# Performance work log

Hardware: AMD Instinct MI355X
Metric: run time of the kernel (lower is better)

Reference implementation:

```python
import jax, jax.numpy as jnp
import numpy as np

DIM = 1024
N_EXPERTS = 8
TOP_K = 2
B, S = 2, 1024


def setup_inputs() -> dict:
    key = jax.random.key(0)
    ks = jax.random.split(key, 4)
    scale = 0.02
    return {
        "u_t": jax.random.normal(ks[0], (B, S, DIM), dtype=jnp.float32),
        "centroids": jax.random.normal(ks[1], (N_EXPERTS, DIM), dtype=jnp.float32),
        "score_biases": jnp.zeros((N_EXPERTS,), dtype=jnp.float32),
        "W1": jax.random.normal(ks[2], (N_EXPERTS, DIM, 4 * DIM), dtype=jnp.float32) * scale,
        "b1": jnp.zeros((N_EXPERTS, 4 * DIM), dtype=jnp.float32),
        "W2": jax.random.normal(ks[3], (N_EXPERTS, 4 * DIM, DIM), dtype=jnp.float32) * scale,
        "b2": jnp.zeros((N_EXPERTS, DIM), dtype=jnp.float32),
    }


def reference(u_t, centroids, score_biases, W1, b1, W2, b2):
    Bs, Ss, dim = u_t.shape
    T = Bs * Ss
    N = centroids.shape[0]
    K = TOP_K

    u_flat = u_t.reshape(T, dim)
    scores = u_flat @ centroids.T + score_biases          # [T, N]
    gate = jax.nn.softmax(scores, axis=-1)                # [T, N]
    topk_vals, topk_idx = jax.lax.top_k(gate, K)          # [T, K]

    flat_idx = topk_idx.reshape(-1)                       # [T*K]

    # load-violation stats (no grad path; pure counts)
    perfect_load = K * T / N
    f_i = jnp.zeros((N,), dtype=jnp.float32).at[flat_idx].add(1.0)
    maxvio = (jnp.max(f_i) - perfect_load) / perfect_load

    # Grouped MLP expressed as dense per-expert compute over all tokens,
    # then combined with a sparse [T, N] gate matrix (same math as masked dispatch).
    h = jax.nn.relu(jnp.einsum("td,ndh->nth", u_flat, W1) + b1[:, None, :])  # [N, T, 4*dim]
    expert_outs = jnp.einsum("nth,nhd->ntd", h, W2) + b2[:, None, :]          # [N, T, dim]

    rows = jnp.repeat(jnp.arange(T), K)
    combine_w = jnp.zeros((T, N), dtype=topk_vals.dtype).at[rows, flat_idx].add(topk_vals.reshape(-1))
    out = jnp.einsum("tn,ntd->td", combine_w, expert_outs).reshape(Bs, Ss, dim)
    return (out, maxvio)
```

## Files before the change

kernel.cpp:

```cpp
#include <hip/hip_runtime.h>
#include <hip/hip_bf16.h>

#define T_TOK 2048
#define DIMS  1024
#define HID   4096
#define NE    8

typedef __bf16 bf16x8 __attribute__((ext_vector_type(8)));
typedef float  f32x4  __attribute__((ext_vector_type(4)));

__device__ __forceinline__ unsigned short f2bf(float f) {
  unsigned u = __float_as_uint(f);
  u += 0x7FFFu + ((u >> 16) & 1u);
  return (unsigned short)(u >> 16);
}

__device__ __forceinline__ void g2l16(const void* g, void* l) {
  __builtin_amdgcn_global_load_lds((const __attribute__((address_space(1))) void*)g,
                                   (__attribute__((address_space(3))) void*)l,
                                   16, 0, 0);
}

__global__ __launch_bounds__(256) void k_zero(int* cnt) {
  if (threadIdx.x < NE) cnt[threadIdx.x] = 0;
}

__global__ __launch_bounds__(256) void k_route(const float* __restrict__ u,
    const float* __restrict__ cent, const float* __restrict__ sbias,
    int* __restrict__ topk_idx, float* __restrict__ topk_val, int* __restrict__ cnt) {
  int wave = threadIdx.x >> 6;
  int lane = threadIdx.x & 63;
  int t = blockIdx.x * 4 + wave;
  const float* ur = u + (size_t)t * DIMS;
  float p[NE];
#pragma unroll
  for (int n = 0; n < NE; n++) p[n] = 0.f;
#pragma unroll
  for (int ch = 0; ch < 4; ch++) {
    int d = ch * 256 + lane * 4;
    float4 uv = *(const float4*)(ur + d);
#pragma unroll
    for (int n = 0; n < NE; n++) {
      float4 cv = *(const float4*)(cent + n * DIMS + d);
      p[n] += uv.x * cv.x + uv.y * cv.y + uv.z * cv.z + uv.w * cv.w;
    }
  }
#pragma unroll
  for (int n = 0; n < NE; n++) {
#pragma unroll
    for (int o = 32; o > 0; o >>= 1) p[n] += __shfl_xor(p[n], o);
  }
  if (lane == 0) {
    float g[NE];
    float m = -1e30f;
#pragma unroll
    for (int n = 0; n < NE; n++) { g[n] = p[n] + sbias[n]; m = fmaxf(m, g[n]); }
    float sum = 0.f;
#pragma unroll
    for (int n = 0; n < NE; n++) { g[n] = expf(g[n] - m); sum += g[n]; }
    float inv = 1.f / sum;
#pragma unroll
    for (int n = 0; n < NE; n++) g[n] *= inv;
    int i0 = 0;
#pragma unroll
    for (int n = 1; n < NE; n++) if (g[n] > g[i0]) i0 = n;
    int i1 = (i0 == 0) ? 1 : 0;
#pragma unroll
    for (int n = 0; n < NE; n++) if (n != i0 && g[n] > g[i1]) i1 = n;
    topk_idx[2 * t] = i0;     topk_idx[2 * t + 1] = i1;
    topk_val[2 * t] = g[i0];  topk_val[2 * t + 1] = g[i1];
    atomicAdd(&cnt[i0], 1);
    atomicAdd(&cnt[i1], 1);
  }
}

__global__ __launch_bounds__(64) void k_finalize(const int* __restrict__ cnt,
    int* __restrict__ offs, int* __restrict__ cursor, float* __restrict__ maxvio) {
  if (threadIdx.x == 0) {
    int o = 0, mx = 0;
#pragma unroll
    for (int n = 0; n < NE; n++) { offs[n] = o; o += cnt[n]; mx = max(mx, cnt[n]); }
    maxvio[0] = ((float)mx - 512.f) / 512.f;
#pragma unroll
    for (int n = 0; n < NE; n++) cursor[n] = 0;
  }
}

__global__ __launch_bounds__(256) void k_place(const int* __restrict__ topk_idx,
    const int* __restrict__ offs, int* __restrict__ cursor,
    int* __restrict__ rowtok, int* __restrict__ pairpos) {
  int t = blockIdx.x * 256 + threadIdx.x;
  if (t >= T_TOK) return;
#pragma unroll
  for (int k = 0; k < 2; k++) {
    int e = topk_idx[2 * t + k];
    int pos = atomicAdd(&cursor[e], 1);
    rowtok[offs[e] + pos] = t;
    pairpos[2 * t + k] = offs[e] + pos;
  }
}

__global__ __launch_bounds__(256) void k_cvt_u(const float* __restrict__ u,
                                               unsigned short* __restrict__ ub) {
  int i = (blockIdx.x * 256 + threadIdx.x) * 8;
  float4 a = *(const float4*)(u + i);
  float4 b = *(const float4*)(u + i + 4);
  union { unsigned short us[8]; uint4 v; } r;
  r.us[0] = f2bf(a.x); r.us[1] = f2bf(a.y); r.us[2] = f2bf(a.z); r.us[3] = f2bf(a.w);
  r.us[4] = f2bf(b.x); r.us[5] = f2bf(b.y); r.us[6] = f2bf(b.z); r.us[7] = f2bf(b.w);
  *(uint4*)(ub + i) = r.v;
}

__global__ __launch_bounds__(256) void k_cvt_w(const float* __restrict__ W,
    unsigned short* __restrict__ out, int R, int C) {
  __shared__ float tile[64][65];
  int e = blockIdx.z;
  size_t base = (size_t)e * R * C;
  int r0 = blockIdx.y * 64, c0 = blockIdx.x * 64;
  int tr  = threadIdx.x >> 4;
  int tc4 = (threadIdx.x & 15) * 4;
#pragma unroll
  for (int it = 0; it < 4; it++) {
    int row = tr + it * 16;
    float4 v = *(const float4*)(W + base + (size_t)(r0 + row) * C + c0 + tc4);
    tile[row][tc4] = v.x; tile[row][tc4 + 1] = v.y; tile[row][tc4 + 2] = v.z; tile[row][tc4 + 3] = v.w;
  }
  __syncthreads();
  int c = threadIdx.x >> 2;
  int seg = (threadIdx.x & 3) * 16;
  union { unsigned short us[8]; uint4 v; } r;
#pragma unroll
  for (int half = 0; half < 2; half++) {
#pragma unroll
    for (int i = 0; i < 8; i++) r.us[i] = f2bf(tile[seg + half * 8 + i][c]);
    *(uint4*)(out + base + (size_t)(c0 + c) * R + r0 + seg + half * 8) = r.v;
  }
}

#define BM 128
#define BN 128
#define BK 64

__global__ __launch_bounds__(256) void k_gemm1(const unsigned short* __restrict__ ub,
    const unsigned short* __restrict__ w1t, const float* __restrict__ b1,
    const int* __restrict__ rowtok, const int* __restrict__ cnts, const int* __restrict__ offs,
    unsigned short* __restrict__ h) {
  int e = blockIdx.z;
  int cnt = cnts[e];
  int m0 = blockIdx.y * BM;
  if (m0 >= cnt) return;
  int off = offs[e];
  int n0 = blockIdx.x * BN;
  __shared__ __align__(16) unsigned char smem[32768];

  int tid = threadIdx.x;
  int lane = tid & 63;
  int wm = (tid >> 7) & 1;
  int wn = (tid >> 6) & 1;
  int srow = tid >> 3;
  int cp = tid & 7;
  const unsigned short* gA[4];
  const unsigned short* gB[4];
#pragma unroll
  for (int a = 0; a < 4; a++) {
    int r = a * 32 + srow;
    int c = cp ^ (r & 7);
    int pr = min(off + m0 + r, off + cnt - 1);
    int tok = rowtok[pr];
    gA[a] = ub + (size_t)tok * DIMS + c * 8;
    gB[a] = w1t + ((size_t)e * HID + (n0 + r)) * DIMS + c * 8;
  }
  int wboff = __builtin_amdgcn_readfirstlane((tid >> 6) << 10);
  f32x4 acc[4][4];
  f32x4 zz = {0.f, 0.f, 0.f, 0.f};
#pragma unroll
  for (int i = 0; i < 4; i++)
#pragma unroll
    for (int j = 0; j < 4; j++) acc[i][j] = zz;

  int lane15 = lane & 15, quad = lane >> 4, l7 = lane & 7;
  unsigned aRowOff = (unsigned)((wm * 64 + lane15) * 128);
  unsigned bRowOff = (unsigned)(16384 + (wn * 64 + lane15) * 128);

#pragma unroll 1
  for (int k0 = 0; k0 < DIMS; k0 += BK) {
#pragma unroll
    for (int a = 0; a < 4; a++) g2l16(gA[a] + k0, smem + a * 4096 + wboff);
#pragma unroll
    for (int a = 0; a < 4; a++) g2l16(gB[a] + k0, smem + 16384 + a * 4096 + wboff);
    __syncthreads();
#pragma unroll
    for (int s = 0; s < 2; s++) {
      unsigned cpf = (unsigned)(((s * 4 + quad) ^ l7) * 16);
      bf16x8 af[4], bfr[4];
#pragma unroll
      for (int i = 0; i < 4; i++) af[i] = *(const bf16x8*)(smem + aRowOff + i * 2048 + cpf);
#pragma unroll
      for (int j = 0; j < 4; j++) bfr[j] = *(const bf16x8*)(smem + bRowOff + j * 2048 + cpf);
#pragma unroll
      for (int i = 0; i < 4; i++)
#pragma unroll
        for (int j = 0; j < 4; j++)
          acc[i][j] = __builtin_amdgcn_mfma_f32_16x16x32_bf16(af[i], bfr[j], acc[i][j], 0, 0, 0);
    }
    __syncthreads();
  }
  float b1v[4];
#pragma unroll
  for (int j = 0; j < 4; j++) b1v[j] = b1[e * HID + n0 + wn * 64 + j * 16 + lane15];
#pragma unroll
  for (int i = 0; i < 4; i++) {
#pragma unroll
    for (int r = 0; r < 4; r++) {
      int mrow = m0 + wm * 64 + i * 16 + quad * 4 + r;
      if (mrow < cnt) {
        size_t hrow = (size_t)(off + mrow) * HID;
#pragma unroll
        for (int j = 0; j < 4; j++) {
          int col = n0 + wn * 64 + j * 16 + lane15;
          float v = fmaxf(acc[i][j][r] + b1v[j], 0.f);
          h[hrow + col] = f2bf(v);
        }
      }
    }
  }
}

__global__ __launch_bounds__(256) void k_gemm2(const unsigned short* __restrict__ hbuf,
    const unsigned short* __restrict__ w2t, const float* __restrict__ b2,
    const int* __restrict__ cnts, const int* __restrict__ offs,
    float* __restrict__ pout, int KC) {
  int z = blockIdx.z;
  int e = z & 7;
  int sp = z >> 3;
  int cnt = cnts[e];
  int m0 = blockIdx.y * BM;
  if (m0 >= cnt) return;
  int off = offs[e];
  int n0 = blockIdx.x * BN;
  __shared__ __align__(16) unsigned char smem[32768];

  int tid = threadIdx.x;
  int lane = tid & 63;
  int wm = (tid >> 7) & 1;
  int wn = (tid >> 6) & 1;
  int srow = tid >> 3;
  int cp = tid & 7;
  const unsigned short* gA[4];
  const unsigned short* gB[4];
#pragma unroll
  for (int a = 0; a < 4; a++) {
    int r = a * 32 + srow;
    int c = cp ^ (r & 7);
    int pr = min(off + m0 + r, off + cnt - 1);
    gA[a] = hbuf + (size_t)pr * HID + c * 8;
    gB[a] = w2t + ((size_t)e * DIMS + (n0 + r)) * HID + c * 8;
  }
  int wboff = __builtin_amdgcn_readfirstlane((tid >> 6) << 10);
  f32x4 acc[4][4];
  f32x4 zz = {0.f, 0.f, 0.f, 0.f};
#pragma unroll
  for (int i = 0; i < 4; i++)
#pragma unroll
    for (int j = 0; j < 4; j++) acc[i][j] = zz;

  int lane15 = lane & 15, quad = lane >> 4, l7 = lane & 7;
  unsigned aRowOff = (unsigned)((wm * 64 + lane15) * 128);
  unsigned bRowOff = (unsigned)(16384 + (wn * 64 + lane15) * 128);

  int kbeg = sp * KC, kend = kbeg + KC;
#pragma unroll 1
  for (int k0 = kbeg; k0 < kend; k0 += BK) {
#pragma unroll
    for (int a = 0; a < 4; a++) g2l16(gA[a] + k0, smem + a * 4096 + wboff);
#pragma unroll
    for (int a = 0; a < 4; a++) g2l16(gB[a] + k0, smem + 16384 + a * 4096 + wboff);
    __syncthreads();
#pragma unroll
    for (int s = 0; s < 2; s++) {
      unsigned cpf = (unsigned)(((s * 4 + quad) ^ l7) * 16);
      bf16x8 af[4], bfr[4];
#pragma unroll
      for (int i = 0; i < 4; i++) af[i] = *(const bf16x8*)(smem + aRowOff + i * 2048 + cpf);
#pragma unroll
      for (int j = 0; j < 4; j++) bfr[j] = *(const bf16x8*)(smem + bRowOff + j * 2048 + cpf);
#pragma unroll
      for (int i = 0; i < 4; i++)
#pragma unroll
        for (int j = 0; j < 4; j++)
          acc[i][j] = __builtin_amdgcn_mfma_f32_16x16x32_bf16(af[i], bfr[j], acc[i][j], 0, 0, 0);
    }
    __syncthreads();
  }
  float b2v[4];
#pragma unroll
  for (int j = 0; j < 4; j++)
    b2v[j] = (sp == 0) ? b2[e * DIMS + n0 + wn * 64 + j * 16 + lane15] : 0.f;
  float* pme = pout + (size_t)sp * T_TOK * 2 * DIMS;
#pragma unroll
  for (int i = 0; i < 4; i++) {
#pragma unroll
    for (int r = 0; r < 4; r++) {
      int mrow = m0 + wm * 64 + i * 16 + quad * 4 + r;
      if (mrow < cnt) {
        size_t prow = (size_t)(off + mrow) * DIMS;
#pragma unroll
        for (int j = 0; j < 4; j++) {
          int col = n0 + wn * 64 + j * 16 + lane15;
          pme[prow + col] = acc[i][j][r] + b2v[j];
        }
      }
    }
  }
}

__global__ __launch_bounds__(256) void k_combine(const float* __restrict__ pout,
    const int* __restrict__ pairpos, const float* __restrict__ tkv,
    float* __restrict__ out, int nsplit) {
  int t = blockIdx.x;
  int d = threadIdx.x * 4;
  int p0 = pairpos[2 * t], p1 = pairpos[2 * t + 1];
  float w0 = tkv[2 * t], w1 = tkv[2 * t + 1];
  float4 a = {0.f, 0.f, 0.f, 0.f}, b = {0.f, 0.f, 0.f, 0.f};
  const size_t SSTRIDE = (size_t)T_TOK * 2 * DIMS;
  for (int s = 0; s < nsplit; s++) {
    float4 av = *(const float4*)(pout + s * SSTRIDE + (size_t)p0 * DIMS + d);
    float4 bv = *(const float4*)(pout + s * SSTRIDE + (size_t)p1 * DIMS + d);
    a.x += av.x; a.y += av.y; a.z += av.z; a.w += av.w;
    b.x += bv.x; b.y += bv.y; b.z += bv.z; b.w += bv.w;
  }
  float4 o;
  o.x = w0 * a.x + w1 * b.x;
  o.y = w0 * a.y + w1 * b.y;
  o.z = w0 * a.z + w1 * b.z;
  o.w = w0 * a.w + w1 * b.w;
  *(float4*)(out + (size_t)t * DIMS + d) = o;
}

extern "C" void kernel_launch(void* const* d_in, const int* in_sizes, int n_in,
                              void* d_out, int out_size, void* d_ws, size_t ws_size,
                              hipStream_t stream) {
  const float* u     = (const float*)d_in[0];
  const float* cent  = (const float*)d_in[1];
  const float* sbias = (const float*)d_in[2];
  const float* W1    = (const float*)d_in[3];
  const float* b1    = (const float*)d_in[4];
  const float* W2    = (const float*)d_in[5];
  const float* b2    = (const float*)d_in[6];
  float* out = (float*)d_out;

  char* ws = (char*)d_ws;
  unsigned short* wT   = (unsigned short*)(ws);
  unsigned short* ubuf = (unsigned short*)(ws + 67108864);
  unsigned short* hbuf = (unsigned short*)(ws + 71303168);
  const size_t POUT_OFF = 104857600ull;
  const size_t PSZ = (size_t)T_TOK * 2 * DIMS * 4;
  int nsplit = (ws_size >= POUT_OFF + 4 * PSZ + (1u << 20)) ? 4 : 1;
  float* pout4 = (float*)(ws + POUT_OFF);
  char* r = ws + POUT_OFF + (size_t)nsplit * PSZ;
  int*   cnt      = (int*)(r);
  int*   offs     = (int*)(r + 64);
  int*   cursor   = (int*)(r + 128);
  int*   topk_idx = (int*)(r + 256);
  float* topk_val = (float*)(r + 256 + 16384);
  int*   rowtok   = (int*)(r + 256 + 32768);
  int*   pairpos  = (int*)(r + 256 + 49152);

  k_zero<<<1, 256, 0, stream>>>(cnt);
  k_route<<<512, 256, 0, stream>>>(u, cent, sbias, topk_idx, topk_val, cnt);
  k_finalize<<<1, 64, 0, stream>>>(cnt, offs, cursor, out + 2097152);
  k_place<<<8, 256, 0, stream>>>(topk_idx, offs, cursor, rowtok, pairpos);
  k_cvt_u<<<1024, 256, 0, stream>>>(u, ubuf);
  k_cvt_w<<<dim3(64, 16, 8), 256, 0, stream>>>(W1, wT, 1024, 4096);
  k_gemm1<<<dim3(32, 16, 8), 256, 0, stream>>>(ubuf, wT, b1, rowtok, cnt, offs, hbuf);
  k_cvt_w<<<dim3(16, 64, 8), 256, 0, stream>>>(W2, wT, 4096, 1024);
  k_gemm2<<<dim3(8, 16, 8 * nsplit), 256, 0, stream>>>(hbuf, wT, b2, cnt, offs,
                                                       pout4, HID / nsplit);
  k_combine<<<2048, 256, 0, stream>>>(pout4, pairpos, topk_val, out, nsplit);
}
```

Before: 504.9 us.

## Fuse conversions, merge weight transposes, count on-chip, store bf16 partials

Folds the fp32-to-bf16 conversion of u into the routing kernel, and merges the two weight transpose-convert launches into one kernel that uses register transposes instead of an LDS tile. Expert counts are now built in a single-block shared-memory histogram, which removes the zero kernel and the global atomics. The split-K partial outputs of the second GEMM are stored as bf16 instead of fp32, halving combine traffic at some cost in accuracy. Fewer launches and less memory traffic are the intended gains. The new transpose does strided per-lane loads, which may be less coalesced than before.

```diff
diff --git a/kernel.cpp b/kernel.cpp
--- a/kernel.cpp
+++ b/kernel.cpp
@@ -14,6 +14,9 @@
   u += 0x7FFFu + ((u >> 16) & 1u);
   return (unsigned short)(u >> 16);
 }
+__device__ __forceinline__ float bf2f(unsigned short s) {
+  return __uint_as_float(((unsigned)s) << 16);
+}
 
 __device__ __forceinline__ void g2l16(const void* g, void* l) {
   __builtin_amdgcn_global_load_lds((const __attribute__((address_space(1))) void*)g,
@@ -21,13 +24,10 @@
                                    16, 0, 0);
 }
 
-__global__ __launch_bounds__(256) void k_zero(int* cnt) {
-  if (threadIdx.x < NE) cnt[threadIdx.x] = 0;
-}
-
 __global__ __launch_bounds__(256) void k_route(const float* __restrict__ u,
     const float* __restrict__ cent, const float* __restrict__ sbias,
-    int* __restrict__ topk_idx, float* __restrict__ topk_val, int* __restrict__ cnt) {
+    int* __restrict__ topk_idx, float* __restrict__ topk_val,
+    unsigned short* __restrict__ ub) {
   int wave = threadIdx.x >> 6;
   int lane = threadIdx.x & 63;
   int t = blockIdx.x * 4 + wave;
@@ -39,6 +39,9 @@
   for (int ch = 0; ch < 4; ch++) {
     int d = ch * 256 + lane * 4;
     float4 uv = *(const float4*)(ur + d);
+    ushort4 o4;
+    o4.x = f2bf(uv.x); o4.y = f2bf(uv.y); o4.z = f2bf(uv.z); o4.w = f2bf(uv.w);
+    *(ushort4*)(ub + (size_t)t * DIMS + d) = o4;
 #pragma unroll
     for (int n = 0; n < NE; n++) {
       float4 cv = *(const float4*)(cent + n * DIMS + d);
@@ -69,20 +72,30 @@
     for (int n = 0; n < NE; n++) if (n != i0 && g[n] > g[i1]) i1 = n;
     topk_idx[2 * t] = i0;     topk_idx[2 * t + 1] = i1;
     topk_val[2 * t] = g[i0];  topk_val[2 * t + 1] = g[i1];
-    atomicAdd(&cnt[i0], 1);
-    atomicAdd(&cnt[i1], 1);
-  }
-}
-
-__global__ __launch_bounds__(64) void k_finalize(const int* __restrict__ cnt,
-    int* __restrict__ offs, int* __restrict__ cursor, float* __restrict__ maxvio) {
+  }
+}
+
+__global__ __launch_bounds__(256) void k_finalize(const int* __restrict__ topk_idx,
+    int* __restrict__ cnt, int* __restrict__ offs, int* __restrict__ cursor,
+    float* __restrict__ maxvio) {
+  __shared__ int lc[NE];
+  if (threadIdx.x < NE) lc[threadIdx.x] = 0;
+  __syncthreads();
+#pragma unroll
+  for (int i = 0; i < 16; i++) {
+    int e = topk_idx[threadIdx.x * 16 + i];
+    atomicAdd(&lc[e], 1);
+  }
+  __syncthreads();
   if (threadIdx.x == 0) {
     int o = 0, mx = 0;
 #pragma unroll
-    for (int n = 0; n < NE; n++) { offs[n] = o; o += cnt[n]; mx = max(mx, cnt[n]); }
+    for (int n = 0; n < NE; n++) {
+      int c = lc[n];
+      cnt[n] = c; offs[n] = o; cursor[n] = 0;
+      o += c; mx = max(mx, c);
+    }
     maxvio[0] = ((float)mx - 512.f) / 512.f;
-#pragma unroll
-    for (int n = 0; n < NE; n++) cursor[n] = 0;
   }
 }
 
@@ -100,40 +113,37 @@
   }
 }
 
-__global__ __launch_bounds__(256) void k_cvt_u(const float* __restrict__ u,
-                                               unsigned short* __restrict__ ub) {
-  int i = (blockIdx.x * 256 + threadIdx.x) * 8;
-  float4 a = *(const float4*)(u + i);
-  float4 b = *(const float4*)(u + i + 4);
-  union { unsigned short us[8]; uint4 v; } r;
-  r.us[0] = f2bf(a.x); r.us[1] = f2bf(a.y); r.us[2] = f2bf(a.z); r.us[3] = f2bf(a.w);
-  r.us[4] = f2bf(b.x); r.us[5] = f2bf(b.y); r.us[6] = f2bf(b.z); r.us[7] = f2bf(b.w);
-  *(uint4*)(ub + i) = r.v;
-}
-
-__global__ __launch_bounds__(256) void k_cvt_w(const float* __restrict__ W,
-    unsigned short* __restrict__ out, int R, int C) {
-  __shared__ float tile[64][65];
-  int e = blockIdx.z;
-  size_t base = (size_t)e * R * C;
-  int r0 = blockIdx.y * 64, c0 = blockIdx.x * 64;
-  int tr  = threadIdx.x >> 4;
-  int tc4 = (threadIdx.x & 15) * 4;
-#pragma unroll
-  for (int it = 0; it < 4; it++) {
-    int row = tr + it * 16;
-    float4 v = *(const float4*)(W + base + (size_t)(r0 + row) * C + c0 + tc4);
-    tile[row][tc4] = v.x; tile[row][tc4 + 1] = v.y; tile[row][tc4 + 2] = v.z; tile[row][tc4 + 3] = v.w;
-  }
-  __syncthreads();
-  int c = threadIdx.x >> 2;
-  int seg = (threadIdx.x & 3) * 16;
-  union { unsigned short us[8]; uint4 v; } r;
-#pragma unroll
-  for (int half = 0; half < 2; half++) {
-#pragma unroll
-    for (int i = 0; i < 8; i++) r.us[i] = f2bf(tile[seg + half * 8 + i][c]);
-    *(uint4*)(out + base + (size_t)(c0 + c) * R + r0 + seg + half * 8) = r.v;
+__global__ __launch_bounds__(256) void k_cvt_w(const float* __restrict__ W1,
+    const float* __restrict__ W2, unsigned short* __restrict__ w1t,
+    unsigned short* __restrict__ w2t) {
+  int bid = blockIdx.x;
+  const float* Wsrc; unsigned short* dst; int R, C, c0, r0b;
+  if (bid < 4096) {
+    int e = bid >> 9, t = bid & 511;
+    R = 1024; C = 4096;
+    c0 = (t & 63) * 64; r0b = (t >> 6) * 128;
+    Wsrc = W1 + (size_t)e * R * C;  dst = w1t + (size_t)e * R * C;
+  } else {
+    int t2 = bid - 4096;
+    int e = t2 >> 9, t = t2 & 511;
+    R = 4096; C = 1024;
+    c0 = (t & 15) * 64; r0b = (t >> 4) * 128;
+    Wsrc = W2 + (size_t)e * R * C;  dst = w2t + (size_t)e * R * C;
+  }
+  int wv = threadIdx.x >> 6, lane = threadIdx.x & 63;
+  int r0 = r0b + wv * 32;
+  int c = c0 + lane;
+  const float* src = Wsrc + (size_t)r0 * C + c;
+  unsigned short rr[32];
+#pragma unroll
+  for (int i = 0; i < 32; i++) rr[i] = f2bf(src[(size_t)i * C]);
+  unsigned short* d = dst + (size_t)c * R + r0;
+  union { unsigned short us[8]; uint4 v; } pk;
+#pragma unroll
+  for (int h = 0; h < 4; h++) {
+#pragma unroll
+    for (int i = 0; i < 8; i++) pk.us[i] = rr[h * 8 + i];
+    *(uint4*)(d + h * 8) = pk.v;
   }
 }
 
@@ -229,7 +239,7 @@
 __global__ __launch_bounds__(256) void k_gemm2(const unsigned short* __restrict__ hbuf,
     const unsigned short* __restrict__ w2t, const float* __restrict__ b2,
     const int* __restrict__ cnts, const int* __restrict__ offs,
-    float* __restrict__ pout, int KC) {
+    unsigned short* __restrict__ pout, int KC) {
   int z = blockIdx.z;
   int e = z & 7;
   int sp = z >> 3;
@@ -296,7 +306,7 @@
 #pragma unroll
   for (int j = 0; j < 4; j++)
     b2v[j] = (sp == 0) ? b2[e * DIMS + n0 + wn * 64 + j * 16 + lane15] : 0.f;
-  float* pme = pout + (size_t)sp * T_TOK * 2 * DIMS;
+  unsigned short* pme = pout + (size_t)sp * T_TOK * 2 * DIMS;
 #pragma unroll
   for (int i = 0; i < 4; i++) {
 #pragma unroll
@@ -307,33 +317,34 @@
 #pragma unroll
         for (int j = 0; j < 4; j++) {
           int col = n0 + wn * 64 + j * 16 + lane15;
-          pme[prow + col] = acc[i][j][r] + b2v[j];
+          pme[prow + col] = f2bf(acc[i][j][r] + b2v[j]);
         }
       }
     }
   }
 }
 
-__global__ __launch_bounds__(256) void k_combine(const float* __restrict__ pout,
+__global__ __launch_bounds__(256) void k_combine(const unsigned short* __restrict__ pout,
     const int* __restrict__ pairpos, const float* __restrict__ tkv,
     float* __restrict__ out, int nsplit) {
   int t = blockIdx.x;
   int d = threadIdx.x * 4;
   int p0 = pairpos[2 * t], p1 = pairpos[2 * t + 1];
   float w0 = tkv[2 * t], w1 = tkv[2 * t + 1];
-  float4 a = {0.f, 0.f, 0.f, 0.f}, b = {0.f, 0.f, 0.f, 0.f};
-  const size_t SSTRIDE = (size_t)T_TOK * 2 * DIMS;
+  float a0 = 0.f, a1 = 0.f, a2 = 0.f, a3 = 0.f;
+  float c0 = 0.f, c1 = 0.f, c2 = 0.f, c3 = 0.f;
+  const size_t SS = (size_t)T_TOK * 2 * DIMS;
   for (int s = 0; s < nsplit; s++) {
-    float4 av = *(const float4*)(pout + s * SSTRIDE + (size_t)p0 * DIMS + d);
-    float4 bv = *(const float4*)(pout + s * SSTRIDE + (size_t)p1 * DIMS + d);
-    a.x += av.x; a.y += av.y; a.z += av.z; a.w += av.w;
-    b.x += bv.x; b.y += bv.y; b.z += bv.z; b.w += bv.w;
+    ushort4 av = *(const ushort4*)(pout + s * SS + (size_t)p0 * DIMS + d);
+    ushort4 bv = *(const ushort4*)(pout + s * SS + (size_t)p1 * DIMS + d);
+    a0 += bf2f(av.x); a1 += bf2f(av.y); a2 += bf2f(av.z); a3 += bf2f(av.w);
+    c0 += bf2f(bv.x); c1 += bf2f(bv.y); c2 += bf2f(bv.z); c3 += bf2f(bv.w);
   }
   float4 o;
-  o.x = w0 * a.x + w1 * b.x;
-  o.y = w0 * a.y + w1 * b.y;
-  o.z = w0 * a.z + w1 * b.z;
-  o.w = w0 * a.w + w1 * b.w;
+  o.x = w0 * a0 + w1 * c0;
+  o.y = w0 * a1 + w1 * c1;
+  o.z = w0 * a2 + w1 * c2;
+  o.w = w0 * a3 + w1 * c3;
   *(float4*)(out + (size_t)t * DIMS + d) = o;
 }
 
@@ -350,13 +361,14 @@
   float* out = (float*)d_out;
 
   char* ws = (char*)d_ws;
-  unsigned short* wT   = (unsigned short*)(ws);
-  unsigned short* ubuf = (unsigned short*)(ws + 67108864);
-  unsigned short* hbuf = (unsigned short*)(ws + 71303168);
-  const size_t POUT_OFF = 104857600ull;
-  const size_t PSZ = (size_t)T_TOK * 2 * DIMS * 4;
+  unsigned short* w1t  = (unsigned short*)(ws);
+  unsigned short* w2t  = (unsigned short*)(ws + 67108864);
+  unsigned short* ubuf = (unsigned short*)(ws + 134217728);
+  unsigned short* hbuf = (unsigned short*)(ws + 138412032);
+  const size_t POUT_OFF = 171966464ull;
+  const size_t PSZ = (size_t)T_TOK * 2 * DIMS * 2;
   int nsplit = (ws_size >= POUT_OFF + 4 * PSZ + (1u << 20)) ? 4 : 1;
-  float* pout4 = (float*)(ws + POUT_OFF);
+  unsigned short* poutb = (unsigned short*)(ws + POUT_OFF);
   char* r = ws + POUT_OFF + (size_t)nsplit * PSZ;
   int*   cnt      = (int*)(r);
   int*   offs     = (int*)(r + 64);
@@ -366,15 +378,12 @@
   int*   rowtok   = (int*)(r + 256 + 32768);
   int*   pairpos  = (int*)(r + 256 + 49152);
 
-  k_zero<<<1, 256, 0, stream>>>(cnt);
-  k_route<<<512, 256, 0, stream>>>(u, cent, sbias, topk_idx, topk_val, cnt);
-  k_finalize<<<1, 64, 0, stream>>>(cnt, offs, cursor, out + 2097152);
+  k_route<<<512, 256, 0, stream>>>(u, cent, sbias, topk_idx, topk_val, ubuf);
+  k_finalize<<<1, 256, 0, stream>>>(topk_idx, cnt, offs, cursor, out + 2097152);
   k_place<<<8, 256, 0, stream>>>(topk_idx, offs, cursor, rowtok, pairpos);
-  k_cvt_u<<<1024, 256, 0, stream>>>(u, ubuf);
-  k_cvt_w<<<dim3(64, 16, 8), 256, 0, stream>>>(W1, wT, 1024, 4096);
-  k_gemm1<<<dim3(32, 16, 8), 256, 0, stream>>>(ubuf, wT, b1, rowtok, cnt, offs, hbuf);
-  k_cvt_w<<<dim3(16, 64, 8), 256, 0, stream>>>(W2, wT, 4096, 1024);
-  k_gemm2<<<dim3(8, 16, 8 * nsplit), 256, 0, stream>>>(hbuf, wT, b2, cnt, offs,
-                                                       pout4, HID / nsplit);
-  k_combine<<<2048, 256, 0, stream>>>(pout4, pairpos, topk_val, out, nsplit);
-}
+  k_cvt_w<<<8192, 256, 0, stream>>>(W1, W2, w1t, w2t);
+  k_gemm1<<<dim3(32, 16, 8), 256, 0, stream>>>(ubuf, w1t, b1, rowtok, cnt, offs, hbuf);
+  k_gemm2<<<dim3(8, 16, 8 * nsplit), 256, 0, stream>>>(hbuf, w2t, b2, cnt, offs,
+                                                       poutb, HID / nsplit);
+  k_combine<<<2048, 256, 0, stream>>>(poutb, pairpos, topk_val, out, nsplit);
+}
```

New measurement: 479.1 us. 5.1% less time.
